# Optimization experiments

Hardware: AMD Instinct MI355X
Metric: run time of the kernel (lower is better)

The kernel has to match this reference:

```python
import jax, jax.numpy as jnp
import numpy as np

H, KVH, D, BS, L = 32, 8, 128, 16, 4096
MAX_BLOCKS = L // BS          # 256 blocks per sequence (sink cache capacity)
B = 16
NUM_BLOCKS = B * MAX_BLOCKS   # 4096 total cache blocks
T = MAX_BLOCKS * BS           # 4096 linearized cache slots per sequence
SCALE = 1.0 / np.sqrt(D)


def _rope_cos_sin(pos):
    # neox-style RoPE tables; pos: int array [...]. returns cos/sin [..., D/2]
    inv_freq = 1.0 / (10000.0 ** (jnp.arange(0, D, 2, dtype=jnp.float32) / D))
    ang = pos[..., None].astype(jnp.float32) * inv_freq
    return jnp.cos(ang), jnp.sin(ang)


def _apply_rope(x, cos, sin):
    # x [..., D]; cos/sin broadcastable to x[..., :D//2]
    x1, x2 = jnp.split(x, 2, axis=-1)
    return jnp.concatenate([x1 * cos - x2 * sin, x2 * cos + x1 * sin], axis=-1)


def setup_inputs() -> dict:
    key = jax.random.key(0)
    ks = jax.random.split(key, 6)
    q = jax.random.normal(ks[0], (B, H * D), dtype=jnp.float32)
    k = jax.random.normal(ks[1], (B, KVH * D), dtype=jnp.float32)
    v = jax.random.normal(ks[2], (B, KVH * D), dtype=jnp.float32)
    key_cache = jax.random.normal(ks[3], (NUM_BLOCKS, BS, KVH, D), dtype=jnp.float32)
    value_cache = jax.random.normal(ks[4], (NUM_BLOCKS, BS, KVH, D), dtype=jnp.float32)
    block_tables = jnp.arange(B * MAX_BLOCKS, dtype=jnp.int32).reshape(B, MAX_BLOCKS)
    context_lens = jax.random.randint(ks[5], (B,), 0, 6000, dtype=jnp.int32)
    return {"q": q, "k": k, "v": v, "key_cache": key_cache,
            "value_cache": value_cache, "block_tables": block_tables,
            "context_lens": context_lens}


def reference(q, k, v, key_cache, value_cache, block_tables, context_lens):
    ctx = context_lens.astype(jnp.int32)                         # [B] past tokens
    rem = ctx % BS
    # sink/rolling cap: if past >= model_context_len, effective seq len caps
    seq_len = jnp.where(ctx >= L, L - BS + rem + 1, ctx + 1)     # [B]
    pos_q = seq_len - 1                                          # capped current position

    # gather pre-rope keys/values from paged cache -> [B, T, KVH, D]
    keys = key_cache[block_tables].reshape(B, T, KVH, D)
    vals = value_cache[block_tables].reshape(B, T, KVH, D)

    # re-apply rope to gathered keys at their cache-relative positions 0..T-1
    cos_k, sin_k = _rope_cos_sin(jnp.arange(T))                  # [T, D/2]
    keys = _apply_rope(keys, cos_k[None, :, None, :], sin_k[None, :, None, :])

    # rope current q, k at capped positions
    cos_q, sin_q = _rope_cos_sin(pos_q)                          # [B, D/2]
    qh = _apply_rope(q.reshape(B, H, D), cos_q[:, None, :], sin_q[:, None, :])
    kh = _apply_rope(k.reshape(B, KVH, D), cos_q[:, None, :], sin_q[:, None, :])

    # scatter current token's k/v at its slot (offset rem in last used block == seq_len-1)
    bidx = jnp.arange(B)
    keys = keys.at[bidx, pos_q].set(kh)
    vals = vals.at[bidx, pos_q].set(v.reshape(B, KVH, D))

    # GQA attention over first seq_len cached tokens
    G = H // KVH
    qg = qh.reshape(B, KVH, G, D)
    scores = jnp.einsum('bhgd,bthd->bhgt', qg, keys) * SCALE     # [B, KVH, G, T]
    mask = jnp.arange(T)[None, :] < seq_len[:, None]             # [B, T]
    scores = jnp.where(mask[:, None, None, :], scores, jnp.finfo(scores.dtype).min)
    probs = jax.nn.softmax(scores, axis=-1)
    out = jnp.einsum('bhgt,bthd->bhgd', probs, vals)             # [B, KVH, G, D]
    return out.reshape(B, H * D)
```

## Files before the change

kernel.cpp:

```cpp
#include <hip/hip_runtime.h>
#include <math.h>

#define B_      16
#define H_      32
#define KVH_    8
#define G_      4
#define D_      128
#define BS_     16
#define L_      4096
#define MAXB_   256
#define T_      4096
#define NPART_  16
#define PART_   256
#define SCALE_  0.08838834764831843f

__device__ __forceinline__ int seq_len_of(int ctx) {
  return (ctx >= L_) ? (L_ - BS_ + (ctx & (BS_ - 1)) + 1) : (ctx + 1);
}

__global__ void rope_table_kernel(float* __restrict__ tab) {
  int idx = blockIdx.x * blockDim.x + threadIdx.x;
  if (idx >= T_ * 64) return;
  int t = idx >> 6, i = idx & 63;
  double inv = pow(10000.0, -(double)(2 * i) / 128.0);
  float ang = (float)t * (float)inv;
  double a = (double)ang;
  tab[2 * idx]     = (float)cos(a);
  tab[2 * idx + 1] = (float)sin(a);
}


#define LOADK(P, tt)                                                        \
  {                                                                         \
    int blk_  = sblk[((tt) - t0) >> 4];                                     \
    int base_ = ((blk_ * BS_ + ((tt) & (BS_ - 1))) * KVH_ + kvh) * D_;      \
    const float4* kc4_ = (const float4*)(kc + base_);                       \
    const float4* vc4_ = (const float4*)(vc + base_);                       \
    P##ka = kc4_[dg];      P##kb = kc4_[16 + dg];                           \
    P##va = vc4_[dg];      P##vb = vc4_[16 + dg];                           \
  }

#define COMPUTE(P, tt)                                                      \
  {                                                                         \
    float kr1[4], kr2[4];                                                   \
    kr1[0] = P##ka.x * cc0.x - P##kb.x * cc0.y;                             \
    kr2[0] = P##kb.x * cc0.x + P##ka.x * cc0.y;                             \
    kr1[1] = P##ka.y * cc0.z - P##kb.y * cc0.w;                             \
    kr2[1] = P##kb.y * cc0.z + P##ka.y * cc0.w;                             \
    kr1[2] = P##ka.z * cc1.x - P##kb.z * cc1.y;                             \
    kr2[2] = P##kb.z * cc1.x + P##ka.z * cc1.y;                             \
    kr1[3] = P##ka.w * cc1.z - P##kb.w * cc1.w;                             \
    kr2[3] = P##kb.w * cc1.z + P##ka.w * cc1.w;                             \
    float4 va_ = P##va, vb_ = P##vb;                                        \
    if ((tt) == posq) {         \
      const float* kp_ = knew + b * (KVH_ * D_) + kvh * D_;                 \
      float4 xa_ = *(const float4*)(kp_ + 4 * dg);                          \
      float4 xb_ = *(const float4*)(kp_ + 64 + 4 * dg);                     \
      float4 p0_ = tab4[posq * 32 + 2 * dg];                                \
      float4 p1_ = tab4[posq * 32 + 2 * dg + 1];                            \
      kr1[0] = xa_.x * p0_.x - xb_.x * p0_.y;                               \
      kr2[0] = xb_.x * p0_.x + xa_.x * p0_.y;                               \
      kr1[1] = xa_.y * p0_.z - xb_.y * p0_.w;                               \
      kr2[1] = xb_.y * p0_.z + xa_.y * p0_.w;                               \
      kr1[2] = xa_.z * p1_.x - xb_.z * p1_.y;                               \
      kr2[2] = xb_.z * p1_.x + xa_.z * p1_.y;                               \
      kr1[3] = xa_.w * p1_.z - xb_.w * p1_.w;                               \
      kr2[3] = xb_.w * p1_.z + xa_.w * p1_.w;                               \
      const float* vp_ = vnew + b * (KVH_ * D_) + kvh * D_;                 \
      va_ = *(const float4*)(vp_ + 4 * dg);                                 \
      vb_ = *(const float4*)(vp_ + 64 + 4 * dg);                            \
    }                                                                       \
    float s[G_];                                                            \
    _Pragma("unroll")                                                       \
    for (int g = 0; g < G_; ++g) {                                          \
      s[g] = kr1[0] * q1[g][0] + kr2[0] * q2[g][0]                          \
           + kr1[1] * q1[g][1] + kr2[1] * q2[g][1]                          \
           + kr1[2] * q1[g][2] + kr2[2] * q2[g][2]                          \
           + kr1[3] * q1[g][3] + kr2[3] * q2[g][3];                         \
    }                                                                       \
    _Pragma("unroll")                                                       \
    for (int off = 1; off <= 8; off <<= 1) {                                \
      _Pragma("unroll")                                                     \
      for (int g = 0; g < G_; ++g) s[g] += __shfl_xor(s[g], off);           \
    }                                                                       \
    _Pragma("unroll")                                                       \
    for (int g = 0; g < G_; ++g) {                                          \
      float sv   = s[g];                                                    \
      float mn   = fmaxf(m[g], sv);                                         \
      float corr = __expf(m[g] - mn);                                       \
      float p    = __expf(sv - mn);                                         \
      m[g] = mn;                                                            \
      l[g] = l[g] * corr + p;                                               \
      acc[g][0] = acc[g][0] * corr + p * va_.x;                             \
      acc[g][1] = acc[g][1] * corr + p * va_.y;                             \
      acc[g][2] = acc[g][2] * corr + p * va_.z;                             \
      acc[g][3] = acc[g][3] * corr + p * va_.w;                             \
      acc[g][4] = acc[g][4] * corr + p * vb_.x;                             \
      acc[g][5] = acc[g][5] * corr + p * vb_.y;                             \
      acc[g][6] = acc[g][6] * corr + p * vb_.z;                             \
      acc[g][7] = acc[g][7] * corr + p * vb_.w;                             \
    }                                                                       \
    {                     \
      float nc_;                                                            \
      nc_ = cc0.x * r0.x - cc0.y * r0.y;                                    \
      cc0.y = cc0.y * r0.x + cc0.x * r0.y; cc0.x = nc_;                     \
      nc_ = cc0.z * r0.z - cc0.w * r0.w;                                    \
      cc0.w = cc0.w * r0.z + cc0.z * r0.w; cc0.z = nc_;                     \
      nc_ = cc1.x * r1.x - cc1.y * r1.y;                                    \
      cc1.y = cc1.y * r1.x + cc1.x * r1.y; cc1.x = nc_;                     \
      nc_ = cc1.z * r1.z - cc1.w * r1.w;                                    \
      cc1.w = cc1.w * r1.z + cc1.z * r1.w; cc1.z = nc_;                     \
    }                                                                       \
  }

__global__ __launch_bounds__(256) void attn_partial_kernel(
    const float* __restrict__ q, const float* __restrict__ knew,
    const float* __restrict__ vnew, const float* __restrict__ kc,
    const float* __restrict__ vc, const int* __restrict__ btab,
    const int* __restrict__ ctxl, const float* __restrict__ tab,
    float* __restrict__ opart, float2* __restrict__ ml) {
  int bid  = blockIdx.x;
  int part = bid & (NPART_ - 1);
  int kvh  = (bid >> 4) & (KVH_ - 1);
  int b    = bid >> 7;

  int seq = seq_len_of(ctxl[b]);
  int t0 = part * PART_;
  if (t0 >= seq) return;
  int t1 = min(t0 + PART_, seq);
  int posq = seq - 1;

  int lane = threadIdx.x & 63;
  int wave = threadIdx.x >> 6;
  int tsub = lane >> 4;
  int dg   = lane & 15;

  __shared__ int sblk[PART_ / BS_];
  if (threadIdx.x < PART_ / BS_)
    sblk[threadIdx.x] = btab[b * MAXB_ + (t0 >> 4) + threadIdx.x];
  __syncthreads();

  const float4* tab4 = (const float4*)tab;

  int tstart = t0 + 4 * wave + tsub;
  float4 cc0 = tab4[tstart * 32 + 2 * dg];
  float4 cc1 = tab4[tstart * 32 + 2 * dg + 1];
  float4 r0  = tab4[16 * 32 + 2 * dg];
  float4 r1  = tab4[16 * 32 + 2 * dg + 1];

  float q1[G_][4], q2[G_][4];
  {
    float4 cq0 = tab4[posq * 32 + 2 * dg];
    float4 cq1 = tab4[posq * 32 + 2 * dg + 1];
#pragma unroll
    for (int g = 0; g < G_; ++g) {
      const float* qp = q + b * (H_ * D_) + (kvh * G_ + g) * D_;
      float4 a  = *(const float4*)(qp + 4 * dg);
      float4 bq = *(const float4*)(qp + 64 + 4 * dg);
      q1[g][0] = (a.x * cq0.x - bq.x * cq0.y) * SCALE_;
      q2[g][0] = (bq.x * cq0.x + a.x * cq0.y) * SCALE_;
      q1[g][1] = (a.y * cq0.z - bq.y * cq0.w) * SCALE_;
      q2[g][1] = (bq.y * cq0.z + a.y * cq0.w) * SCALE_;
      q1[g][2] = (a.z * cq1.x - bq.z * cq1.y) * SCALE_;
      q2[g][2] = (bq.z * cq1.x + a.z * cq1.y) * SCALE_;
      q1[g][3] = (a.w * cq1.z - bq.w * cq1.w) * SCALE_;
      q2[g][3] = (bq.w * cq1.z + a.w * cq1.w) * SCALE_;
    }
  }

  float m[G_], l[G_], acc[G_][8];
#pragma unroll
  for (int g = 0; g < G_; ++g) {
    m[g] = -1e30f; l[g] = 0.f;
#pragma unroll
    for (int j = 0; j < 8; ++j) acc[g][j] = 0.f;
  }

  {
    float4 Aka, Akb, Ava, Avb;
    float4 Bka, Bkb, Bva, Bvb;
    float4 Cka, Ckb, Cva, Cvb;
    int t = t0 + 4 * wave + tsub;
    if (t < t1) {
      LOADK(A, t);
      if (t + 16 < t1) LOADK(B, t + 16);
      while (1) {
        if (t + 32 < t1) LOADK(C, t + 32);
        COMPUTE(A, t);
        t += 16; if (t >= t1) break;
        if (t + 32 < t1) LOADK(A, t + 32);
        COMPUTE(B, t);
        t += 16; if (t >= t1) break;
        if (t + 32 < t1) LOADK(B, t + 32);
        COMPUTE(C, t);
        t += 16; if (t >= t1) break;
      }
    }
  }

  auto merge_off = [&](int off) {
#pragma unroll
    for (int g = 0; g < G_; ++g) {
      float mo = __shfl_xor(m[g], off);
      float lo = __shfl_xor(l[g], off);
      float M  = fmaxf(m[g], mo);
      float fa = __expf(m[g] - M);
      float fb = __expf(mo - M);
      l[g] = l[g] * fa + lo * fb;
      m[g] = M;
#pragma unroll
      for (int j = 0; j < 8; ++j) {
        float ao = __shfl_xor(acc[g][j], off);
        acc[g][j] = acc[g][j] * fa + ao * fb;
      }
    }
  };
  merge_off(16);
  merge_off(32);

  __shared__ float  lds_acc[4][G_][D_];
  __shared__ float2 lds_ml[4][G_];
  if (lane < 16) {
#pragma unroll
    for (int g = 0; g < G_; ++g) {
#pragma unroll
      for (int j = 0; j < 8; ++j) {
        int dim = (j < 4) ? (4 * dg + j) : (64 + 4 * dg + (j - 4));
        lds_acc[wave][g][dim] = acc[g][j];
      }
      if (lane == 0) lds_ml[wave][g] = make_float2(m[g], l[g]);
    }
  }
  __syncthreads();
  if (wave == 0) {
    int w = tsub;
#pragma unroll
    for (int g = 0; g < G_; ++g) {
      float2 t2 = lds_ml[w][g];
      m[g] = t2.x; l[g] = t2.y;
#pragma unroll
      for (int j = 0; j < 8; ++j) {
        int dim = (j < 4) ? (4 * dg + j) : (64 + 4 * dg + (j - 4));
        acc[g][j] = lds_acc[w][g][dim];
      }
    }
    merge_off(16);
    merge_off(32);
    if (lane < 16) {
#pragma unroll
      for (int g = 0; g < G_; ++g) {
        float* op = opart + (size_t)(bid * G_ + g) * D_;
#pragma unroll
        for (int j = 0; j < 8; ++j) {
          int dim = (j < 4) ? (4 * dg + j) : (64 + 4 * dg + (j - 4));
          op[dim] = acc[g][j];
        }
        if (lane == 0) ml[bid * G_ + g] = make_float2(m[g], l[g]);
      }
    }
  }
}

__global__ void attn_reduce_kernel(const float* __restrict__ opart,
                                   const float2* __restrict__ ml,
                                   const int* __restrict__ ctxl,
                                   float* __restrict__ out) {
  int bh = blockIdx.x;
  int b = bh >> 5, h = bh & 31;
  int kvh = h >> 2, g = h & 3;
  int d = threadIdx.x;
  int seq = seq_len_of(ctxl[b]);
  int nlive = (seq + PART_ - 1) / PART_;
  int base = (b * KVH_ + kvh) * NPART_;

  float M = -1e30f;
  for (int p = 0; p < nlive; ++p) M = fmaxf(M, ml[(base + p) * G_ + g].x);
  float L = 0.f, O = 0.f;
  for (int p = 0; p < nlive; ++p) {
    float2 mlv = ml[(base + p) * G_ + g];
    float f = __expf(mlv.x - M);
    L += mlv.y * f;
    O += opart[(size_t)((base + p) * G_ + g) * D_ + d] * f;
  }
  out[b * (H_ * D_) + h * D_ + d] = O / L;
}

extern "C" void kernel_launch(void* const* d_in, const int* in_sizes, int n_in,
                              void* d_out, int out_size, void* d_ws, size_t ws_size,
                              hipStream_t stream) {
  const float* q    = (const float*)d_in[0];
  const float* k    = (const float*)d_in[1];
  const float* v    = (const float*)d_in[2];
  const float* kc   = (const float*)d_in[3];
  const float* vc   = (const float*)d_in[4];
  const int*   btab = (const int*)d_in[5];
  const int*   ctxl = (const int*)d_in[6];
  float* out = (float*)d_out;

  float*  tab   = (float*)d_ws;
  float*  opart = tab + (size_t)T_ * 64 * 2;
  float2* ml    = (float2*)(opart + (size_t)B_ * KVH_ * NPART_ * G_ * D_);

  rope_table_kernel<<<(T_ * 64 + 255) / 256, 256, 0, stream>>>(tab);
  attn_partial_kernel<<<B_ * KVH_ * NPART_, 256, 0, stream>>>(
      q, k, v, kc, vc, btab, ctxl, tab, opart, ml);
  attn_reduce_kernel<<<B_ * H_, D_, 0, stream>>>(opart, ml, ctxl, out);
}
```

Measured before the change: 119.1 us.

## Make the KV loop branch-free with clamped loads, masking, and a 4-stage rotation

Replaces the data-dependent early-exit loop with a fixed trip count (rounded to a multiple of four) over a four-buffer register rotation. Loads are clamped to the last valid token and out-of-range or current-position tokens are masked out of the softmax. The current token's new k/v is handled once after the loop by the 16 lanes holding that position instead of being checked in every iteration. This removes per-iteration branches and keeps loads issued unconditionally ahead of use, at the cost of wasted work on padded tail iterations and more register pressure from the fourth buffer.

```diff
diff --git a/kernel.cpp b/kernel.cpp
--- a/kernel.cpp
+++ b/kernel.cpp
@@ -32,8 +32,9 @@
 
 #define LOADK(P, tt)                                                        \
   {                                                                         \
-    int blk_  = sblk[((tt) - t0) >> 4];                                     \
-    int base_ = ((blk_ * BS_ + ((tt) & (BS_ - 1))) * KVH_ + kvh) * D_;      \
+    int tcl_  = min((tt), t1m1);                                            \
+    int blk_  = sblk[(tcl_ - t0) >> 4];                                     \
+    int base_ = ((blk_ * BS_ + (tcl_ & (BS_ - 1))) * KVH_ + kvh) * D_;      \
     const float4* kc4_ = (const float4*)(kc + base_);                       \
     const float4* vc4_ = (const float4*)(vc + base_);                       \
     P##ka = kc4_[dg];      P##kb = kc4_[16 + dg];                           \
@@ -51,25 +52,7 @@
     kr2[2] = P##kb.z * cc1.x + P##ka.z * cc1.y;                             \
     kr1[3] = P##ka.w * cc1.z - P##kb.w * cc1.w;                             \
     kr2[3] = P##kb.w * cc1.z + P##ka.w * cc1.w;                             \
-    float4 va_ = P##va, vb_ = P##vb;                                        \
-    if ((tt) == posq) {         \
-      const float* kp_ = knew + b * (KVH_ * D_) + kvh * D_;                 \
-      float4 xa_ = *(const float4*)(kp_ + 4 * dg);                          \
-      float4 xb_ = *(const float4*)(kp_ + 64 + 4 * dg);                     \
-      float4 p0_ = tab4[posq * 32 + 2 * dg];                                \
-      float4 p1_ = tab4[posq * 32 + 2 * dg + 1];                            \
-      kr1[0] = xa_.x * p0_.x - xb_.x * p0_.y;                               \
-      kr2[0] = xb_.x * p0_.x + xa_.x * p0_.y;                               \
-      kr1[1] = xa_.y * p0_.z - xb_.y * p0_.w;                               \
-      kr2[1] = xb_.y * p0_.z + xa_.y * p0_.w;                               \
-      kr1[2] = xa_.z * p1_.x - xb_.z * p1_.y;                               \
-      kr2[2] = xb_.z * p1_.x + xa_.z * p1_.y;                               \
-      kr1[3] = xa_.w * p1_.z - xb_.w * p1_.w;                               \
-      kr2[3] = xb_.w * p1_.z + xa_.w * p1_.w;                               \
-      const float* vp_ = vnew + b * (KVH_ * D_) + kvh * D_;                 \
-      va_ = *(const float4*)(vp_ + 4 * dg);                                 \
-      vb_ = *(const float4*)(vp_ + 64 + 4 * dg);                            \
-    }                                                                       \
+    bool valid_ = ((tt) < t1) & ((tt) != posq);                             \
     float s[G_];                                                            \
     _Pragma("unroll")                                                       \
     for (int g = 0; g < G_; ++g) {                                          \
@@ -85,20 +68,21 @@
     }                                                                       \
     _Pragma("unroll")                                                       \
     for (int g = 0; g < G_; ++g) {                                          \
-      float sv   = s[g];                                                    \
+      float sv   = valid_ ? s[g] : -1e30f;                                  \
       float mn   = fmaxf(m[g], sv);                                         \
       float corr = __expf(m[g] - mn);                                       \
       float p    = __expf(sv - mn);                                         \
+      p = valid_ ? p : 0.0f;                                                \
       m[g] = mn;                                                            \
       l[g] = l[g] * corr + p;                                               \
-      acc[g][0] = acc[g][0] * corr + p * va_.x;                             \
-      acc[g][1] = acc[g][1] * corr + p * va_.y;                             \
-      acc[g][2] = acc[g][2] * corr + p * va_.z;                             \
-      acc[g][3] = acc[g][3] * corr + p * va_.w;                             \
-      acc[g][4] = acc[g][4] * corr + p * vb_.x;                             \
-      acc[g][5] = acc[g][5] * corr + p * vb_.y;                             \
-      acc[g][6] = acc[g][6] * corr + p * vb_.z;                             \
-      acc[g][7] = acc[g][7] * corr + p * vb_.w;                             \
+      acc[g][0] = acc[g][0] * corr + p * P##va.x;                           \
+      acc[g][1] = acc[g][1] * corr + p * P##va.y;                           \
+      acc[g][2] = acc[g][2] * corr + p * P##va.z;                           \
+      acc[g][3] = acc[g][3] * corr + p * P##va.w;                           \
+      acc[g][4] = acc[g][4] * corr + p * P##vb.x;                           \
+      acc[g][5] = acc[g][5] * corr + p * P##vb.y;                           \
+      acc[g][6] = acc[g][6] * corr + p * P##vb.z;                           \
+      acc[g][7] = acc[g][7] * corr + p * P##vb.w;                           \
     }                                                                       \
     {                     \
       float nc_;                                                            \
@@ -128,6 +112,7 @@
   int t0 = part * PART_;
   if (t0 >= seq) return;
   int t1 = min(t0 + PART_, seq);
+  int t1m1 = t1 - 1;
   int posq = seq - 1;
 
   int lane = threadIdx.x & 63;
@@ -180,21 +165,63 @@
     float4 Aka, Akb, Ava, Avb;
     float4 Bka, Bkb, Bva, Bvb;
     float4 Cka, Ckb, Cva, Cvb;
-    int t = t0 + 4 * wave + tsub;
-    if (t < t1) {
-      LOADK(A, t);
-      if (t + 16 < t1) LOADK(B, t + 16);
-      while (1) {
-        if (t + 32 < t1) LOADK(C, t + 32);
-        COMPUTE(A, t);
-        t += 16; if (t >= t1) break;
-        if (t + 32 < t1) LOADK(A, t + 32);
-        COMPUTE(B, t);
-        t += 16; if (t >= t1) break;
-        if (t + 32 < t1) LOADK(B, t + 32);
-        COMPUTE(C, t);
-        t += 16; if (t >= t1) break;
-      }
+    float4 Dka, Dkb, Dva, Dvb;
+    int nIter = ((t1 - t0 + 15) >> 4);
+    nIter = (nIter + 3) & ~3;
+    int t = tstart;
+    LOADK(A, t);
+    LOADK(B, t + 16);
+    for (int it = 0; it < nIter; it += 4) {
+      LOADK(C, t + 32);  COMPUTE(A, t);  t += 16;
+      LOADK(D, t + 32);  COMPUTE(B, t);  t += 16;
+      LOADK(A, t + 32);  COMPUTE(C, t);  t += 16;
+      LOADK(B, t + 32);  COMPUTE(D, t);  t += 16;
+    }
+  }
+
+  if (threadIdx.x < 16 && posq >= t0 && posq < t1) {
+    const float* kp = knew + (b * KVH_ + kvh) * D_;
+    float4 xa = *(const float4*)(kp + 4 * dg);
+    float4 xb = *(const float4*)(kp + 64 + 4 * dg);
+    float4 p0 = tab4[posq * 32 + 2 * dg];
+    float4 p1 = tab4[posq * 32 + 2 * dg + 1];
+    float kr1[4], kr2[4];
+    kr1[0] = xa.x * p0.x - xb.x * p0.y;  kr2[0] = xb.x * p0.x + xa.x * p0.y;
+    kr1[1] = xa.y * p0.z - xb.y * p0.w;  kr2[1] = xb.y * p0.z + xa.y * p0.w;
+    kr1[2] = xa.z * p1.x - xb.z * p1.y;  kr2[2] = xb.z * p1.x + xa.z * p1.y;
+    kr1[3] = xa.w * p1.z - xb.w * p1.w;  kr2[3] = xb.w * p1.z + xa.w * p1.w;
+    const float* vp = vnew + (b * KVH_ + kvh) * D_;
+    float4 va_ = *(const float4*)(vp + 4 * dg);
+    float4 vb_ = *(const float4*)(vp + 64 + 4 * dg);
+    float s[G_];
+#pragma unroll
+    for (int g = 0; g < G_; ++g) {
+      s[g] = kr1[0] * q1[g][0] + kr2[0] * q2[g][0]
+           + kr1[1] * q1[g][1] + kr2[1] * q2[g][1]
+           + kr1[2] * q1[g][2] + kr2[2] * q2[g][2]
+           + kr1[3] * q1[g][3] + kr2[3] * q2[g][3];
+    }
+#pragma unroll
+    for (int off = 1; off <= 8; off <<= 1) {
+#pragma unroll
+      for (int g = 0; g < G_; ++g) s[g] += __shfl_xor(s[g], off);
+    }
+#pragma unroll
+    for (int g = 0; g < G_; ++g) {
+      float sv   = s[g];
+      float mn   = fmaxf(m[g], sv);
+      float corr = __expf(m[g] - mn);
+      float p    = __expf(sv - mn);
+      m[g] = mn;
+      l[g] = l[g] * corr + p;
+      acc[g][0] = acc[g][0] * corr + p * va_.x;
+      acc[g][1] = acc[g][1] * corr + p * va_.y;
+      acc[g][2] = acc[g][2] * corr + p * va_.z;
+      acc[g][3] = acc[g][3] * corr + p * va_.w;
+      acc[g][4] = acc[g][4] * corr + p * vb_.x;
+      acc[g][5] = acc[g][5] * corr + p * vb_.y;
+      acc[g][6] = acc[g][6] * corr + p * vb_.z;
+      acc[g][7] = acc[g][7] * corr + p * vb_.w;
     }
   }
 
```

Result: slower. 125.3 us (+5.2%).
